# Performance work log

Hardware: AMD Instinct MI355X
Metric: run time of the kernel (lower is better)

The kernel has to match this reference:

```python
import jax, jax.numpy as jnp
import numpy as np

NUM_NODE = 100000
EMBED_DIM = 128
N_EDGES = 600000


def setup_inputs() -> dict:
    key = jax.random.key(0)
    k1, k2, k3, k4 = jax.random.split(key, 4)
    x = jax.random.normal(k1, (NUM_NODE, EMBED_DIM), dtype=jnp.float32)
    edge_index = jax.random.randint(k2, (2, N_EDGES), 0, NUM_NODE, dtype=jnp.int64)
    # nn.Linear(embed_dim, embed_dim): weight [out, in], bias [out]
    scale = 1.0 / np.sqrt(EMBED_DIM)
    W = jax.random.uniform(k3, (EMBED_DIM, EMBED_DIM), dtype=jnp.float32, minval=-scale, maxval=scale)
    b = jax.random.uniform(k4, (EMBED_DIM,), dtype=jnp.float32, minval=-scale, maxval=scale)
    return {"x": x, "edge_index": edge_index, "W": W, "b": b}


def reference(x, edge_index, W, b):
    source_nodes = edge_index[0]
    target_nodes = edge_index[1]
    # x_target = relu(Linear(x))  -- torch Linear: x @ W.T + b
    x_target = jax.nn.relu(x @ W.T + b)                      # [N, D]
    # scatter-add of gathered target features into source rows
    gathered = x_target[target_nodes]                        # [E, D]
    aggr = jax.ops.segment_sum(gathered, source_nodes, num_segments=NUM_NODE)  # [N, D]
    # degree normalization: bincount clamped to >= 1
    deg = jax.ops.segment_sum(jnp.ones((edge_index.shape[1],), dtype=jnp.float32),
                              source_nodes, num_segments=NUM_NODE)
    deg = jnp.maximum(deg, 1.0)
    return aggr / deg[:, None]
```

## Files before the change

kernel.cpp:

```cpp
#include <hip/hip_runtime.h>
#include <hip/hip_bf16.h>

typedef float f4 __attribute__((ext_vector_type(4)));
typedef float f32x4 __attribute__((ext_vector_type(4)));
typedef short bf16x8 __attribute__((ext_vector_type(8)));

#define D 128
#define SLOTS 64

__device__ __forceinline__ unsigned f2bf_u(float f) {
    unsigned u = __builtin_bit_cast(unsigned, f);
    unsigned r = 0x7FFFu + ((u >> 16) & 1u);
    return (u + r) >> 16;
}
__device__ __forceinline__ unsigned short f2bf(float f) {
    return (unsigned short)f2bf_u(f);
}
__device__ __forceinline__ float bf2f(short s) {
    unsigned u = ((unsigned)(unsigned short)s) << 16;
    return __builtin_bit_cast(float, u);
}

__global__ __launch_bounds__(256) void init_kernel(
    const float* __restrict__ W, unsigned short* __restrict__ Wbf,
    int* __restrict__ deg, int N)
{
    int i = blockIdx.x * 256 + threadIdx.x;
    if (i < D * D / 4) {
        f4 w = reinterpret_cast<const f4*>(W)[i];
        uint2 o;
        o.x = f2bf_u(w[0]) | (f2bf_u(w[1]) << 16);
        o.y = f2bf_u(w[2]) | (f2bf_u(w[3]) << 16);
        *reinterpret_cast<uint2*>(Wbf + i * 4) = o;
    }
    if (i < N) deg[i] = 0;
}

__global__ __launch_bounds__(256, 4) void gemm_mfma(
    const float* __restrict__ x, const unsigned short* __restrict__ Wbf,
    const float* __restrict__ b, unsigned short* __restrict__ ybf, int N)
{
    __shared__ unsigned short Wl[D * D];
    __shared__ float bl[D];

    {
        const int t = threadIdx.x;
        const int r = t >> 1;
        const unsigned hb = (unsigned)((t & 1) * 128);
        const unsigned swz = (unsigned)((r & 7) << 4);
        const char* src = (const char*)Wbf + r * 256;
        char* dst = (char*)Wl + r * 256;
#pragma unroll
        for (int j = 0; j < 8; ++j) {
            unsigned cb = hb + j * 16;
            *reinterpret_cast<uint4*>(dst + cb) =
                *reinterpret_cast<const uint4*>(src + (cb ^ swz));
        }
        if (t < D) bl[t] = b[t];
    }
    __syncthreads();

    const int lane = threadIdx.x & 63;
    const int r16  = lane & 15;
    const int g4   = lane >> 4;

    const int ntiles = (N + 15) >> 4;
    const int tile = blockIdx.x * 4 + (threadIdx.x >> 6);
    if (tile >= ntiles) return;

    int arow = tile * 16 + r16;
    const int srow = (arow < N) ? arow : N - 1;
    const float* xr = x + (size_t)srow * D + g4 * 8;

    f4 xa[4][2];
#pragma unroll
    for (int kf = 0; kf < 4; ++kf) {
        xa[kf][0] = *reinterpret_cast<const f4*>(xr + kf * 32);
        xa[kf][1] = *reinterpret_cast<const f4*>(xr + kf * 32 + 4);
    }
    union { bf16x8 v; unsigned short s[8]; } afrag[4];
#pragma unroll
    for (int kf = 0; kf < 4; ++kf)
#pragma unroll
        for (int e = 0; e < 8; ++e)
            afrag[kf].s[e] = f2bf(e < 4 ? xa[kf][0][e] : xa[kf][1][e - 4]);

    const unsigned rbase = (unsigned)(r16 * 256);
    const unsigned rswz  = (unsigned)((r16 & 7) << 4);
    const unsigned gcb   = (unsigned)(g4 * 16);

    unsigned short* yrow = ybf + (size_t)arow * D + g4 * 4;
#pragma unroll 2
    for (int ct = 0; ct < 8; ++ct) {
        bf16x8 wf[4];
#pragma unroll
        for (int kf = 0; kf < 4; ++kf) {
            unsigned off = (unsigned)(ct * 4096) + rbase
                         + (((unsigned)(kf * 64) + gcb) ^ rswz);
            wf[kf] = *reinterpret_cast<const bf16x8*>((const char*)Wl + off);
        }
        f32x4 acc = {0.f, 0.f, 0.f, 0.f};
#pragma unroll
        for (int kf = 0; kf < 4; ++kf)
            acc = __builtin_amdgcn_mfma_f32_16x16x32_bf16(
                wf[kf], afrag[kf].v, acc, 0, 0, 0);
        if (arow < N) {
            f4 bias = *reinterpret_cast<const f4*>(bl + ct * 16 + g4 * 4);
            float v0 = fmaxf(acc[0] + bias[0], 0.f);
            float v1 = fmaxf(acc[1] + bias[1], 0.f);
            float v2 = fmaxf(acc[2] + bias[2], 0.f);
            float v3 = fmaxf(acc[3] + bias[3], 0.f);
            uint2 o;
            o.x = f2bf_u(v0) | (f2bf_u(v1) << 16);
            o.y = f2bf_u(v2) | (f2bf_u(v3) << 16);
            *reinterpret_cast<uint2*>(yrow + 16 * ct) = o;
        }
    }
}

__global__ __launch_bounds__(256) void scatter_hist_kernel(
    const int* __restrict__ src, const int* __restrict__ tgt,
    int* __restrict__ deg, int* __restrict__ slot, int E)
{
    int e = blockIdx.x * 256 + threadIdx.x;
    if (e < E) {
        int s = src[e];
        int p = atomicAdd(&deg[s], 1);
        slot[(size_t)s * SLOTS + p] = tgt[e];
    }
}

__global__ __launch_bounds__(256) void aggregate_bf16(
    const int* __restrict__ deg, const int* __restrict__ slot,
    const unsigned short* __restrict__ ybf, float* __restrict__ out, int N)
{
    const int g  = threadIdx.x >> 4;
    const int c8 = (threadIdx.x & 15) * 8;

    const int n = blockIdx.x * 16 + g;
    if (n >= N) return;
    const int d = deg[n];
    const int* sl = slot + (size_t)n * SLOTS;

    float a0[8] = {0,0,0,0,0,0,0,0}, a1[8] = {0,0,0,0,0,0,0,0};
    float a2[8] = {0,0,0,0,0,0,0,0}, a3[8] = {0,0,0,0,0,0,0,0};

    for (int j = 0; j < d; j += 4) {
        int4 tq = *reinterpret_cast<const int4*>(sl + j);
        if (j + 0 < d) {
            bf16x8 v = *reinterpret_cast<const bf16x8*>(ybf + (size_t)tq.x * D + c8);
#pragma unroll
            for (int e = 0; e < 8; ++e) a0[e] += bf2f(v[e]);
        }
        if (j + 1 < d) {
            bf16x8 v = *reinterpret_cast<const bf16x8*>(ybf + (size_t)tq.y * D + c8);
#pragma unroll
            for (int e = 0; e < 8; ++e) a1[e] += bf2f(v[e]);
        }
        if (j + 2 < d) {
            bf16x8 v = *reinterpret_cast<const bf16x8*>(ybf + (size_t)tq.z * D + c8);
#pragma unroll
            for (int e = 0; e < 8; ++e) a2[e] += bf2f(v[e]);
        }
        if (j + 3 < d) {
            bf16x8 v = *reinterpret_cast<const bf16x8*>(ybf + (size_t)tq.w * D + c8);
#pragma unroll
            for (int e = 0; e < 8; ++e) a3[e] += bf2f(v[e]);
        }
    }

    const float dinv = 1.0f / fmaxf((float)d, 1.f);
    f4 o0, o1;
#pragma unroll
    for (int e = 0; e < 4; ++e)
        o0[e] = ((a0[e] + a1[e]) + (a2[e] + a3[e])) * dinv;
#pragma unroll
    for (int e = 4; e < 8; ++e)
        o1[e - 4] = ((a0[e] + a1[e]) + (a2[e] + a3[e])) * dinv;

    float* orow = out + (size_t)n * D + c8;
    *reinterpret_cast<f4*>(orow)     = o0;
    *reinterpret_cast<f4*>(orow + 4) = o1;
}

extern "C" void kernel_launch(void* const* d_in, const int* in_sizes, int n_in,
                              void* d_out, int out_size, void* d_ws, size_t ws_size,
                              hipStream_t stream) {
    const float* x  = (const float*)d_in[0];
    const int*   ei = (const int*)d_in[1];
    const float* W  = (const float*)d_in[2];
    const float* b  = (const float*)d_in[3];
    float* out = (float*)d_out;

    const int N = in_sizes[0] / D;
    const int E = in_sizes[1] / 2;
    const int* src = ei;
    const int* tgt = ei + E;

    char* ws = (char*)d_ws;
    unsigned short* ybf = (unsigned short*)ws;   ws += (size_t)N * D * sizeof(unsigned short);
    unsigned short* Wbf = (unsigned short*)ws;   ws += (size_t)D * D * sizeof(unsigned short);
    int* deg  = (int*)ws;                        ws += (size_t)N * sizeof(int);
    int* slot = (int*)ws;                        ws += (size_t)N * SLOTS * sizeof(int);

    int ib = (N + 255) / 256;
    init_kernel<<<ib, 256, 0, stream>>>(W, Wbf, deg, N);

    int ntiles = (N + 15) / 16;
    int gb = (ntiles + 3) / 4;
    gemm_mfma<<<gb, 256, 0, stream>>>(x, Wbf, b, ybf, N);

    int eb = (E + 255) / 256;
    scatter_hist_kernel<<<eb, 256, 0, stream>>>(src, tgt, deg, slot, E);

    int ab = (N + 15) / 16;
    aggregate_bf16<<<ab, 256, 0, stream>>>(deg, slot, ybf, out, N);
}
```

Measured before the change: 93.97 us.

## Fuse GEMM and edge scatter into one persistent kernel with register-held weights

The GEMM and the edge slot-scatter kernels are merged into a single persistent kernel launched on a fixed 1024-block grid. In the GEMM part, each wave now keeps two column tiles of W in registers loaded straight from global memory, so the LDS staging and __syncthreads go away. The four waves of a block split the 128 output columns of each 16-row tile and loop over tiles in grid-stride fashion. This removes one launch and the shared-memory weight traffic, and lets the atomics overlap with the MFMA work, at the cost of each x tile being loaded by four waves and a fixed grid size.

```diff
diff --git a/kernel.cpp b/kernel.cpp
--- a/kernel.cpp
+++ b/kernel.cpp
@@ -36,94 +36,75 @@
     if (i < N) deg[i] = 0;
 }
 
-__global__ __launch_bounds__(256, 4) void gemm_mfma(
+__global__ __launch_bounds__(256, 4) void gemm_scatter(
     const float* __restrict__ x, const unsigned short* __restrict__ Wbf,
-    const float* __restrict__ b, unsigned short* __restrict__ ybf, int N)
+    const float* __restrict__ b, unsigned short* __restrict__ ybf,
+    const int* __restrict__ src, const int* __restrict__ tgt,
+    int* __restrict__ deg, int* __restrict__ slot, int N, int E)
 {
-    __shared__ unsigned short Wl[D * D];
-    __shared__ float bl[D];
-
-    {
-        const int t = threadIdx.x;
-        const int r = t >> 1;
-        const unsigned hb = (unsigned)((t & 1) * 128);
-        const unsigned swz = (unsigned)((r & 7) << 4);
-        const char* src = (const char*)Wbf + r * 256;
-        char* dst = (char*)Wl + r * 256;
-#pragma unroll
-        for (int j = 0; j < 8; ++j) {
-            unsigned cb = hb + j * 16;
-            *reinterpret_cast<uint4*>(dst + cb) =
-                *reinterpret_cast<const uint4*>(src + (cb ^ swz));
-        }
-        if (t < D) bl[t] = b[t];
-    }
-    __syncthreads();
-
     const int lane = threadIdx.x & 63;
     const int r16  = lane & 15;
     const int g4   = lane >> 4;
+    const int ct0  = (threadIdx.x >> 6) * 2;
+
+    bf16x8 wfrag[2][4];
+#pragma unroll
+    for (int c = 0; c < 2; ++c)
+#pragma unroll
+        for (int kf = 0; kf < 4; ++kf)
+            wfrag[c][kf] = *reinterpret_cast<const bf16x8*>(
+                Wbf + (size_t)(16 * (ct0 + c) + r16) * D + kf * 32 + g4 * 8);
+
+    f4 bias[2];
+#pragma unroll
+    for (int c = 0; c < 2; ++c)
+        bias[c] = *reinterpret_cast<const f4*>(b + 16 * (ct0 + c) + g4 * 4);
 
     const int ntiles = (N + 15) >> 4;
-    const int tile = blockIdx.x * 4 + (threadIdx.x >> 6);
-    if (tile >= ntiles) return;
+    for (int tile = blockIdx.x; tile < ntiles; tile += gridDim.x) {
+        const int arow = tile * 16 + r16;
+        const int srow = (arow < N) ? arow : N - 1;
+        const float* xr = x + (size_t)srow * D + g4 * 8;
 
-    int arow = tile * 16 + r16;
-    const int srow = (arow < N) ? arow : N - 1;
-    const float* xr = x + (size_t)srow * D + g4 * 8;
-
-    f4 xa[4][2];
-#pragma unroll
-    for (int kf = 0; kf < 4; ++kf) {
-        xa[kf][0] = *reinterpret_cast<const f4*>(xr + kf * 32);
-        xa[kf][1] = *reinterpret_cast<const f4*>(xr + kf * 32 + 4);
-    }
-    union { bf16x8 v; unsigned short s[8]; } afrag[4];
-#pragma unroll
-    for (int kf = 0; kf < 4; ++kf)
-#pragma unroll
-        for (int e = 0; e < 8; ++e)
-            afrag[kf].s[e] = f2bf(e < 4 ? xa[kf][0][e] : xa[kf][1][e - 4]);
-
-    const unsigned rbase = (unsigned)(r16 * 256);
-    const unsigned rswz  = (unsigned)((r16 & 7) << 4);
-    const unsigned gcb   = (unsigned)(g4 * 16);
-
-    unsigned short* yrow = ybf + (size_t)arow * D + g4 * 4;
-#pragma unroll 2
-    for (int ct = 0; ct < 8; ++ct) {
-        bf16x8 wf[4];
+        union { bf16x8 v; unsigned short s[8]; } afrag[4];
 #pragma unroll
         for (int kf = 0; kf < 4; ++kf) {
-            unsigned off = (unsigned)(ct * 4096) + rbase
-                         + (((unsigned)(kf * 64) + gcb) ^ rswz);
-            wf[kf] = *reinterpret_cast<const bf16x8*>((const char*)Wl + off);
+            f4 x0 = *reinterpret_cast<const f4*>(xr + kf * 32);
+            f4 x1 = *reinterpret_cast<const f4*>(xr + kf * 32 + 4);
+#pragma unroll
+            for (int e = 0; e < 4; ++e) {
+                afrag[kf].s[e]     = f2bf(x0[e]);
+                afrag[kf].s[e + 4] = f2bf(x1[e]);
+            }
         }
-        f32x4 acc = {0.f, 0.f, 0.f, 0.f};
+
+        f32x4 acc0 = {0.f, 0.f, 0.f, 0.f};
+        f32x4 acc1 = {0.f, 0.f, 0.f, 0.f};
 #pragma unroll
-        for (int kf = 0; kf < 4; ++kf)
-            acc = __builtin_amdgcn_mfma_f32_16x16x32_bf16(
-                wf[kf], afrag[kf].v, acc, 0, 0, 0);
+        for (int kf = 0; kf < 4; ++kf) {
+            acc0 = __builtin_amdgcn_mfma_f32_16x16x32_bf16(
+                wfrag[0][kf], afrag[kf].v, acc0, 0, 0, 0);
+            acc1 = __builtin_amdgcn_mfma_f32_16x16x32_bf16(
+                wfrag[1][kf], afrag[kf].v, acc1, 0, 0, 0);
+        }
+
         if (arow < N) {
-            f4 bias = *reinterpret_cast<const f4*>(bl + ct * 16 + g4 * 4);
-            float v0 = fmaxf(acc[0] + bias[0], 0.f);
-            float v1 = fmaxf(acc[1] + bias[1], 0.f);
-            float v2 = fmaxf(acc[2] + bias[2], 0.f);
-            float v3 = fmaxf(acc[3] + bias[3], 0.f);
-            uint2 o;
-            o.x = f2bf_u(v0) | (f2bf_u(v1) << 16);
-            o.y = f2bf_u(v2) | (f2bf_u(v3) << 16);
-            *reinterpret_cast<uint2*>(yrow + 16 * ct) = o;
+            unsigned short* yrow = ybf + (size_t)arow * D + g4 * 4;
+            uint2 o0, o1;
+            o0.x = f2bf_u(fmaxf(acc0[0] + bias[0][0], 0.f))
+                 | (f2bf_u(fmaxf(acc0[1] + bias[0][1], 0.f)) << 16);
+            o0.y = f2bf_u(fmaxf(acc0[2] + bias[0][2], 0.f))
+                 | (f2bf_u(fmaxf(acc0[3] + bias[0][3], 0.f)) << 16);
+            o1.x = f2bf_u(fmaxf(acc1[0] + bias[1][0], 0.f))
+                 | (f2bf_u(fmaxf(acc1[1] + bias[1][1], 0.f)) << 16);
+            o1.y = f2bf_u(fmaxf(acc1[2] + bias[1][2], 0.f))
+                 | (f2bf_u(fmaxf(acc1[3] + bias[1][3], 0.f)) << 16);
+            *reinterpret_cast<uint2*>(yrow + 16 * ct0)        = o0;
+            *reinterpret_cast<uint2*>(yrow + 16 * (ct0 + 1))  = o1;
         }
     }
-}
 
-__global__ __launch_bounds__(256) void scatter_hist_kernel(
-    const int* __restrict__ src, const int* __restrict__ tgt,
-    int* __restrict__ deg, int* __restrict__ slot, int E)
-{
-    int e = blockIdx.x * 256 + threadIdx.x;
-    if (e < E) {
+    for (int e = blockIdx.x * 256 + threadIdx.x; e < E; e += gridDim.x * 256) {
         int s = src[e];
         int p = atomicAdd(&deg[s], 1);
         slot[(size_t)s * SLOTS + p] = tgt[e];
@@ -206,12 +187,8 @@
     int ib = (N + 255) / 256;
     init_kernel<<<ib, 256, 0, stream>>>(W, Wbf, deg, N);
 
-    int ntiles = (N + 15) / 16;
-    int gb = (ntiles + 3) / 4;
-    gemm_mfma<<<gb, 256, 0, stream>>>(x, Wbf, b, ybf, N);
-
-    int eb = (E + 255) / 256;
-    scatter_hist_kernel<<<eb, 256, 0, stream>>>(src, tgt, deg, slot, E);
+    gemm_scatter<<<1024, 256, 0, stream>>>(x, Wbf, b, ybf, src, tgt,
+                                           deg, slot, N, E);
 
     int ab = (N + 15) / 16;
     aggregate_bf16<<<ab, 256, 0, stream>>>(deg, slot, ybf, out, N);
```

Result: faster. 89.09 us (-5.2%).
